# Kernel optimization log

Measured on AMD Instinct MI355X. Metric: run time of the kernel, lower is better.

The kernel has to match this reference:

```python
import jax, jax.numpy as jnp
import numpy as np

DN = ('NCHW', 'OIHW', 'NCHW')

def _conv(x, W, pad):
    return jax.lax.conv_general_dilated(x, W, (1, 1), [(pad, pad), (pad, pad)], dimension_numbers=DN)

def _cbs(x, W, s, b, pad):
    # Conv2d(bias=False) + folded BatchNorm (scale/bias) + SiLU
    y = _conv(x, W, pad) * s[None, :, None, None] + b[None, :, None, None]
    return y * jax.nn.sigmoid(y)

def _l2norm(x):
    n = jnp.sqrt(jnp.sum(x * x, axis=1, keepdims=True))
    return x / jnp.maximum(n, 1e-12)

def setup_inputs() -> dict:
    key = jax.random.key(0)
    ks = jax.random.split(key, 24)
    B, C, H, L, TD, NC = 16, 256, 64, 40, 768, 8
    EMB = (TD + NC * 2) // 2  # 392
    w = lambda k, sh: jax.random.normal(k, sh, jnp.float32) * 0.02
    img = jax.random.normal(ks[0], (B, C, H, H), jnp.float32)
    flang = jax.random.normal(ks[1], (B, L, TD), jnp.float32)
    lengths = jax.random.randint(ks[2], (B, 1), 5, L + 1)
    word_mask = (jnp.arange(L)[None, :] < lengths).astype(jnp.int32)
    return {
        'img': img, 'flang': flang, 'word_mask': word_mask, 'sigma_w': 0.1,
        'W1': w(ks[3], (EMB, TD)), 'b1': w(ks[4], (EMB,)),
        'W2': w(ks[5], (NC * 2, EMB)), 'b2': w(ks[6], (NC * 2,)),
        'Wv': w(ks[7], (C, C, 1, 1)), 'sv': jnp.ones((C,)), 'bv': w(ks[8], (C,)),
        'Wg': w(ks[9], (NC, NC, 1, 1)), 'sg': jnp.ones((NC,)), 'bg': w(ks[10], (NC,)),
        'Wb': w(ks[11], (NC, NC, 1, 1)), 'sb': jnp.ones((NC,)), 'bb': w(ks[12], (NC,)),
        'Wf1': w(ks[13], (C, C, 1, 1)), 'sf1': jnp.ones((C,)), 'bf1': w(ks[14], (C,)),
        'Wf2': w(ks[15], (C, C, 3, 3)), 'sf2': jnp.ones((C,)), 'bf2': w(ks[16], (C,)),
        'Wf3': w(ks[17], (C, C, 1, 1)), 'bf3': w(ks[18], (C,)),
        'Ws': w(ks[19], (NC, C, 3, 3)), 'bs': w(ks[20], (NC,)),
        'add_weight': jnp.zeros((), jnp.float32),
    }

def reference(img, flang, word_mask, sigma_w, W1, b1, W2, b2, Wv, sv, bv,
              Wg, sg, bg, Wb, sb, bb, Wf1, sf1, bf1, Wf2, sf2, bf2,
              Wf3, bf3, Ws, bs, add_weight):
    B, C, H = img.shape[0], img.shape[1], img.shape[2]
    nc = Wg.shape[0]
    map_visu = jnp.tanh(_cbs(img, Wv, sv, bv, 0))
    # ragged masked mean excluding first (CLS) and last (SEP) masked tokens
    m = word_mask.astype(jnp.float32)
    c = jnp.cumsum(m, axis=1)
    tot = c[:, -1:]
    inc = m * ((c > 1) & (c < tot)).astype(jnp.float32)  # [B,L]
    flang_avg = jnp.sum(flang * inc[:, :, None], axis=1) / jnp.sum(inc, axis=1, keepdims=True)
    map_flang = jax.nn.sigmoid((flang_avg @ W1.T + b1) @ W2.T + b2)  # [B,2*nc]
    maps = map_flang.reshape(B, nc, 2)
    sigma_x = sigma_w * H
    sig = _conv(img, Ws, 0) + bs[None, :, None, None]  # [B,nc,H-2,H-2]
    sigma_weight = jax.nn.sigmoid(jnp.mean(sig, axis=(2, 3), keepdims=True))  # [B,nc,1,1]
    sigma_y = sigma_x * sigma_weight
    yc = (maps[:, :, 0] * H).astype(jnp.int32).astype(jnp.float32)[:, :, None, None]
    xc = (maps[:, :, 1] * H).astype(jnp.int32).astype(jnp.float32)[:, :, None, None]
    gy = jnp.arange(H, dtype=jnp.float32)[None, None, :, None]
    gx = jnp.arange(H, dtype=jnp.float32)[None, None, None, :]
    weights = jnp.exp(-((gy - yc) ** 2 / (2.0 * sigma_y ** 2) + (gx - xc) ** 2 / (2.0 * sigma_x ** 2)))  # [B,nc,H,H]
    gamma = jnp.tanh(_cbs(weights, Wg, sg, bg, 0))
    beta = jnp.tanh(_cbs(weights, Wb, sb, bb, 0))
    g = jnp.mean(gamma, axis=1, keepdims=True)
    bmax = jnp.max(beta, axis=1, keepdims=True)
    v_film = _l2norm(g * map_visu + bmax)
    v_film = _cbs(v_film, Wf1, sf1, bf1, 0)
    v_film = _cbs(v_film, Wf2, sf2, bf2, 1)
    v_film = _conv(v_film, Wf3, 0) + bf3[None, :, None, None]
    aw = jnp.tanh(add_weight)
    v_add = (1.0 + aw) * img + (1.0 - aw) * v_film
    return _l2norm(v_add)
```

## Files before the change

kernel.cpp:

```cpp
#include <hip/hip_runtime.h>
#include <hip/hip_bf16.h>


#define DEVFN static __device__ __forceinline__

DEVFN float sigmoidf_(float x) { return 1.f / (1.f + expf(-x)); }
DEVFN float siluf_(float y) { return y / (1.f + __expf(-y)); }
DEVFN float tanh_fast_(float x) { return 1.f - 2.f / (__expf(2.f * x) + 1.f); }

typedef __attribute__((ext_vector_type(8))) short bf16x8;
typedef __attribute__((ext_vector_type(4))) float f32x4;

DEVFN unsigned short f2bf_(float f) {
    union { __hip_bfloat16 b; unsigned short u; } cv;
    cv.b = __float2bfloat16(f);
    return cv.u;
}
DEVFN float bf2f_(unsigned short u) {
    union { unsigned short u; __hip_bfloat16 b; } cv;
    cv.u = u;
    return __bfloat162float(cv.b);
}

DEVFN void async_cp16(const void* g, void* l) {
    __builtin_amdgcn_global_load_lds(
        (const __attribute__((address_space(1))) unsigned int*)g,
        (__attribute__((address_space(3))) unsigned int*)l, 16, 0, 0);
}

#define M1_LANG_END 16
#define M1_WSUM_END 1040
#define M1_GRID     1680

__global__ __launch_bounds__(256) void mega1_kernel(
        const float* __restrict__ Wv, const float* __restrict__ Wf1,
        const float* __restrict__ Wf3, const float* __restrict__ Wf2,
        short* __restrict__ WvB, short* __restrict__ W1B,
        short* __restrict__ W3B, short* __restrict__ WB2,
        float* __restrict__ zbuf,
        const float* __restrict__ img, float* __restrict__ S,
        const float* __restrict__ flang, const int* __restrict__ mask,
        const float* __restrict__ Wm1, const float* __restrict__ bm1,
        const float* __restrict__ Wm2, const float* __restrict__ bm2,
        float* __restrict__ ycxc) {
    __shared__ int   mlds[40];
    __shared__ float inc[40];
    __shared__ float isum;
    __shared__ __attribute__((aligned(16))) float fa[768];
    __shared__ float h[392];
    __shared__ float o16[16];
    int bid = blockIdx.x, t = threadIdx.x;
    int w = t >> 6, lane = t & 63;

    if (bid < M1_LANG_END) {
        int b = bid;
        if (t < 40) mlds[t] = mask[b * 40 + t];
        __syncthreads();
        if (t == 0) {
            float cum = 0.f;
            float tot = 0.f;
            for (int l = 0; l < 40; ++l) tot += (float)mlds[l];
            float sm = 0.f;
            for (int l = 0; l < 40; ++l) {
                float m = (float)mlds[l];
                cum += m;
                float v = (cum > 1.f && cum < tot) ? m : 0.f;
                inc[l] = v; sm += v;
            }
            isum = sm;
        }
        __syncthreads();
        {
            float rinv = 1.f / isum;
            for (int d = t; d < 768; d += 256) {
                float a = 0.f;
                const float* fp = flang + (size_t)(b * 40) * 768 + d;
                for (int l = 0; l < 40; ++l) a = fmaf(fp[(size_t)l * 768], inc[l], a);
                fa[d] = a * rinv;
            }
        }
        __syncthreads();
        {
            const float4* W14 = (const float4*)Wm1;
            const float4* fa4 = (const float4*)fa;
            for (int u = w; u < 392; u += 4) {
                float a = 0.f;
#pragma unroll
                for (int j = 0; j < 3; ++j) {
                    float4 wv = W14[(size_t)u * 192 + j * 64 + lane];
                    float4 fv = fa4[j * 64 + lane];
                    a = fmaf(wv.x, fv.x, a);
                    a = fmaf(wv.y, fv.y, a);
                    a = fmaf(wv.z, fv.z, a);
                    a = fmaf(wv.w, fv.w, a);
                }
#pragma unroll
                for (int m = 32; m; m >>= 1) a += __shfl_xor(a, m);
                if (lane == 0) h[u] = a + bm1[u];
            }
        }
        __syncthreads();
        {
#pragma unroll
            for (int q = 0; q < 4; ++q) {
                int u2 = w * 4 + q;
                float a = 0.f;
#pragma unroll
                for (int j = 0; j < 7; ++j) {
                    int k = j * 64 + lane;
                    if (k < 392) a = fmaf(h[k], Wm2[(size_t)u2 * 392 + k], a);
                }
#pragma unroll
                for (int m = 32; m; m >>= 1) a += __shfl_xor(a, m);
                if (lane == 0) o16[u2] = sigmoidf_(a + bm2[u2]);
            }
        }
        __syncthreads();
        if (t < 8) {
            ycxc[b * 8 + t]       = (float)(int)(o16[2 * t] * 64.f);
            ycxc[128 + b * 8 + t] = (float)(int)(o16[2 * t + 1] * 64.f);
        }
    } else if (bid < M1_WSUM_END) {
        int bc = (bid - M1_LANG_END) * 4 + w;
        const float4* p4 = (const float4*)(img + (size_t)bc * 4096);
        int lx2 = lane & 15;
        float s[9];
#pragma unroll
        for (int k = 0; k < 9; ++k) s[k] = 0.f;
#pragma unroll
        for (int i = 0; i < 16; ++i) {
            float4 v = p4[lane + i * 64];
            int y = (lane >> 4) + 4 * i;
            float sum4 = v.x + v.y + v.z + v.w;
            float p0 = (lx2 == 15) ? (v.x + v.y) : sum4;
            float p1 = sum4 - ((lx2 == 0) ? v.x : 0.f)
                            - ((lx2 == 15) ? v.w : 0.f);
            float p2 = (lx2 == 0) ? (v.z + v.w) : sum4;
            float ym0 = (y <= 61) ? 1.f : 0.f;
            float ym1 = (y >= 1 && y <= 62) ? 1.f : 0.f;
            float ym2 = (y >= 2) ? 1.f : 0.f;
            s[0] = fmaf(ym0, p0, s[0]); s[1] = fmaf(ym0, p1, s[1]); s[2] = fmaf(ym0, p2, s[2]);
            s[3] = fmaf(ym1, p0, s[3]); s[4] = fmaf(ym1, p1, s[4]); s[5] = fmaf(ym1, p2, s[5]);
            s[6] = fmaf(ym2, p0, s[6]); s[7] = fmaf(ym2, p1, s[7]); s[8] = fmaf(ym2, p2, s[8]);
        }
#pragma unroll
        for (int m = 32; m; m >>= 1)
#pragma unroll
            for (int k = 0; k < 9; ++k) s[k] += __shfl_xor(s[k], m);
        if (lane == 0) {
#pragma unroll
            for (int k = 0; k < 9; ++k) S[(size_t)bc * 9 + k] = s[k];
        }
    } else {
        int base = (bid - M1_WSUM_END) * 1024;
#pragma unroll
        for (int i = 0; i < 4; ++i) {
            int idx = base + i * 256 + t;
            if (idx < 8) zbuf[idx] = 0.f;
            if (idx < 65536) {
                int j    = idx & 7;
                int ln   = (idx >> 3) & 63;
                int coT  = (idx >> 9) & 15;
                int ci32 = (idx >> 13) & 7;
                int co = coT * 16 + (ln & 15);
                int ci = ci32 * 32 + ((ln >> 4) << 3) + j;
                int src = co * 256 + ci;
                WvB[idx] = (short)f2bf_(Wv[src]);
                W1B[idx] = (short)f2bf_(Wf1[src]);
                W3B[idx] = (short)f2bf_(Wf3[src]);
            }
            int oo = idx - 65536;
            if (oo >= 0 && oo < 589824) {
                int j    = oo & 7;
                int ln   = (oo >> 3) & 63;
                int coT  = (oo >> 9) & 15;
                int ci32 = (oo >> 13) & 7;
                int kk   = oo >> 16;
                int co = coT * 16 + (ln & 15);
                int ci = ci32 * 32 + ((ln >> 4) << 3) + j;
                WB2[oo] = (short)f2bf_(Wf2[(co * 256 + ci) * 9 + kk]);
            }
        }
    }
}

__global__ __launch_bounds__(256) void f01_kernel(
        const float* __restrict__ img, const short* __restrict__ wvb,
        const short* __restrict__ w1b,
        const float* __restrict__ sv, const float* __restrict__ bv,
        const float* __restrict__ s1, const float* __restrict__ b1,
        const float* __restrict__ S, const float* __restrict__ Ws,
        const float* __restrict__ bs, const float* __restrict__ ycxc,
        const float* __restrict__ sigma_w,
        const float* __restrict__ Wg, const float* __restrict__ sg,
        const float* __restrict__ bg,
        const float* __restrict__ Wb, const float* __restrict__ sb,
        const float* __restrict__ bb,
        __hip_bfloat16* __restrict__ outB) {
    __shared__ __attribute__((aligned(16))) short lA[64 * 264];
    __shared__ float invs[64];
    __shared__ float ls_sv[256], ls_bv[256], ls_s1[256], ls_b1[256];
    __shared__ float ls_g[64], ls_bm[64];
    __shared__ float sigw8[8];
    float* red = (float*)lA;
    float* pr  = (float*)lA;
    int blk = blockIdx.x, b = blk >> 6, y = blk & 63;
    int t = threadIdx.x, w = t >> 6, lane = t & 63;
    int lx = lane & 15, koct = lane >> 4;

    ls_sv[t] = sv[t]; ls_bv[t] = bv[t];
    ls_s1[t] = s1[t]; ls_b1[t] = b1[t];

    {
        float s9[9];
        const float* Sp = S + (size_t)(b * 256 + t) * 9;
#pragma unroll
        for (int k = 0; k < 9; ++k) s9[k] = Sp[k];
#pragma unroll
        for (int co = 0; co < 8; ++co) {
            const float* wp = Ws + (size_t)(co * 256 + t) * 9;
            float a = 0.f;
#pragma unroll
            for (int k = 0; k < 9; ++k) a = fmaf(wp[k], s9[k], a);
            red[co * 256 + t] = a;
        }
        __syncthreads();
        for (int st = 128; st > 0; st >>= 1) {
            if (t < st) {
#pragma unroll
                for (int co = 0; co < 8; ++co) red[co * 256 + t] += red[co * 256 + t + st];
            }
            __syncthreads();
        }
        if (t < 8) sigw8[t] = sigmoidf_(red[t * 256] / 3844.f + bs[t]);
        __syncthreads();
    }

    if (t < 64) {
        float sx = sigma_w[0] * 64.f;
        float wv8[8];
#pragma unroll
        for (int n = 0; n < 8; ++n) {
            float yc = ycxc[b * 8 + n], xc = ycxc[128 + b * 8 + n];
            float sy = sx * sigw8[n];
            float dy = (float)y - yc, dx = (float)t - xc;
            wv8[n] = expf(-(dy * dy / (2.f * sy * sy) + dx * dx / (2.f * sx * sx)));
        }
        float gacc = 0.f, bmax = -3.4e38f;
#pragma unroll
        for (int n = 0; n < 8; ++n) {
            float a1 = 0.f, a2 = 0.f;
#pragma unroll
            for (int m = 0; m < 8; ++m) {
                a1 = fmaf(Wg[n * 8 + m], wv8[m], a1);
                a2 = fmaf(Wb[n * 8 + m], wv8[m], a2);
            }
            float ga = tanhf(siluf_(a1 * sg[n] + bg[n]));
            float be = tanhf(siluf_(a2 * sb[n] + bb[n]));
            gacc += ga;
            bmax = fmaxf(bmax, be);
        }
        ls_g[t]  = gacc * 0.125f;
        ls_bm[t] = bmax;
    }

    {
        int x = t & 63, cg = t >> 6;
        const float* ib = img + (size_t)b * 1048576 + y * 64 + x;
#pragma unroll
        for (int c8 = 0; c8 < 8; ++c8) {
            int ci0 = cg * 64 + c8 * 8;
            unsigned short r[8];
#pragma unroll
            for (int j = 0; j < 8; ++j) r[j] = f2bf_(ib[(size_t)(ci0 + j) * 4096]);
            *(uint4*)&lA[x * 264 + ci0] = *(uint4*)r;
        }
    }
    f32x4 acc[4][4];
#pragma unroll
    for (int mi = 0; mi < 4; ++mi)
#pragma unroll
        for (int ni = 0; ni < 4; ++ni) acc[mi][ni] = (f32x4){0.f, 0.f, 0.f, 0.f};
    __syncthreads();

#pragma unroll
    for (int k32 = 0; k32 < 8; ++k32) {
        const short* wp = wvb + (((k32 * 16) + w * 4) * 64 + lane) * 8;
        bf16x8 bfr[4];
#pragma unroll
        for (int ni = 0; ni < 4; ++ni) bfr[ni] = *(const bf16x8*)(wp + ni * 512);
        bf16x8 afr[4];
#pragma unroll
        for (int mi = 0; mi < 4; ++mi)
            afr[mi] = *(const bf16x8*)&lA[(mi * 16 + lx) * 264 + k32 * 32 + koct * 8];
#pragma unroll
        for (int mi = 0; mi < 4; ++mi)
#pragma unroll
            for (int ni = 0; ni < 4; ++ni)
                acc[mi][ni] = __builtin_amdgcn_mfma_f32_16x16x32_bf16(afr[mi], bfr[ni], acc[mi][ni], 0, 0, 0);
    }
    __syncthreads();

#pragma unroll
    for (int mi = 0; mi < 4; ++mi)
#pragma unroll
        for (int rr = 0; rr < 4; ++rr) {
            int x = mi * 16 + koct * 4 + rr;
            float ps = 0.f;
#pragma unroll
            for (int ni = 0; ni < 4; ++ni) {
                int co = w * 64 + ni * 16 + lx;
                float yv = fmaf(acc[mi][ni][rr], ls_sv[co], ls_bv[co]);
                float mvv = tanh_fast_(siluf_(yv));
                float v = fmaf(ls_g[x], mvv, ls_bm[x]);
                acc[mi][ni][rr] = v;
                ps += v * v;
            }
            pr[x * 64 + w * 16 + lx] = ps;
        }
    __syncthreads();
    if (t < 64) {
        float s2 = 0.f;
        for (int q = 0; q < 64; ++q) s2 += pr[t * 64 + q];
        invs[t] = 1.f / fmaxf(sqrtf(s2), 1e-12f);
    }
    __syncthreads();

#pragma unroll
    for (int mi = 0; mi < 4; ++mi)
#pragma unroll
        for (int ni = 0; ni < 4; ++ni) {
            int co = w * 64 + ni * 16 + lx;
#pragma unroll
            for (int rr = 0; rr < 4; ++rr) {
                int x = mi * 16 + koct * 4 + rr;
                lA[x * 264 + co] = (short)f2bf_(acc[mi][ni][rr] * invs[x]);
            }
        }
#pragma unroll
    for (int mi = 0; mi < 4; ++mi)
#pragma unroll
        for (int ni = 0; ni < 4; ++ni) acc[mi][ni] = (f32x4){0.f, 0.f, 0.f, 0.f};
    __syncthreads();

#pragma unroll
    for (int k32 = 0; k32 < 8; ++k32) {
        const short* wp = w1b + (((k32 * 16) + w * 4) * 64 + lane) * 8;
        bf16x8 bfr[4];
#pragma unroll
        for (int ni = 0; ni < 4; ++ni) bfr[ni] = *(const bf16x8*)(wp + ni * 512);
        bf16x8 afr[4];
#pragma unroll
        for (int mi = 0; mi < 4; ++mi)
            afr[mi] = *(const bf16x8*)&lA[(mi * 16 + lx) * 264 + k32 * 32 + koct * 8];
#pragma unroll
        for (int mi = 0; mi < 4; ++mi)
#pragma unroll
            for (int ni = 0; ni < 4; ++ni)
                acc[mi][ni] = __builtin_amdgcn_mfma_f32_16x16x32_bf16(afr[mi], bfr[ni], acc[mi][ni], 0, 0, 0);
    }
    __syncthreads();

#pragma unroll
    for (int mi = 0; mi < 4; ++mi)
#pragma unroll
        for (int ni = 0; ni < 4; ++ni) {
            int co = w * 64 + ni * 16 + lx;
#pragma unroll
            for (int rr = 0; rr < 4; ++rr) {
                int x = mi * 16 + koct * 4 + rr;
                float yv = fmaf(acc[mi][ni][rr], ls_s1[co], ls_b1[co]);
                lA[x * 264 + co] = (short)f2bf_(siluf_(yv));
            }
        }
    __syncthreads();
    unsigned short* og = (unsigned short*)outB + (size_t)(b * 64 + y) * 16384;
#pragma unroll
    for (int it = 0; it < 8; ++it) {
        int e8 = t + it * 256;
        int x2 = e8 >> 5, c8 = e8 & 31;
        *(uint4*)(og + e8 * 8) = *(uint4*)&lA[x2 * 264 + c8 * 8];
    }
}

DEVFN void stage_chunk(const unsigned short* __restrict__ xg, short* ldsbuf,
                       const unsigned short* __restrict__ zbuf, int cc, int y0, int t) {
#pragma unroll
    for (int p = 0; p < 10; ++p) {
        int slot = t + p * 256;
        if (slot < 2376) {
            int r = slot / 594;
            int rem = slot - r * 594;
            int xp = rem / 9;
            int oct = rem - xp * 9;
            int ys = y0 + r - 1, xs = xp - 1;
            bool valid = (oct < 8) && (ys >= 0) && (ys < 64) && (xs >= 0) && (xs < 64);
            const unsigned short* gp = valid ? (xg + ((ys * 64 + xs) * 256 + cc * 64 + oct * 8))
                                             : zbuf;
            async_cp16(gp, ldsbuf + slot * 8);
        }
    }
}

__global__ __launch_bounds__(256, 2) void c3f_kernel(const __hip_bfloat16* __restrict__ xin,
                                                     const short* __restrict__ wb,
                                                     const float* __restrict__ sc,
                                                     const float* __restrict__ bi,
                                                     const float* __restrict__ zbufF,
                                                     const short* __restrict__ w3b,
                                                     const float* __restrict__ bf3,
                                                     const float* __restrict__ img,
                                                     const float* __restrict__ addw,
                                                     float* __restrict__ outF) {
    __shared__ __attribute__((aligned(16))) short lds[2][19008];
    __shared__ float pr2[256];
    __shared__ float invs[64];
    __shared__ float ls_b3[256];
    int blk = blockIdx.x;
    int b = blk >> 5, y0 = (blk & 31) * 2;
    int t = threadIdx.x;
    int w = t >> 6, lane = t & 63;
    int lx = lane & 15, koct = lane >> 4;
    const unsigned short* xg = (const unsigned short*)xin + (size_t)b * 1048576;
    const unsigned short* zbuf = (const unsigned short*)zbufF;
    ls_b3[t] = bf3[t];

    f32x4 acc[8][4];
#pragma unroll
    for (int mi = 0; mi < 8; ++mi)
#pragma unroll
        for (int ni = 0; ni < 4; ++ni) acc[mi][ni] = (f32x4){0.f, 0.f, 0.f, 0.f};

    stage_chunk(xg, lds[0], zbuf, 0, y0, t);
    __syncthreads();

    for (int cc = 0; cc < 4; ++cc) {
        short* cur = lds[cc & 1];
        if (cc < 3) stage_chunk(xg, lds[(cc + 1) & 1], zbuf, cc + 1, y0, t);
        for (int kk = 0; kk < 9; ++kk) {
            int ky = kk / 3, kx = kk - ky * 3;
#pragma unroll
            for (int k32 = 0; k32 < 2; ++k32) {
                const short* wp = wb + ((((kk * 8 + cc * 2 + k32) * 16) + w * 4) * 64 + lane) * 8;
                bf16x8 bfr[4];
#pragma unroll
                for (int ni = 0; ni < 4; ++ni)
                    bfr[ni] = *(const bf16x8*)(wp + ni * 512);
                bf16x8 afr[8];
#pragma unroll
                for (int mi = 0; mi < 8; ++mi) {
                    int row = mi >> 2, xb = (mi & 3) * 16;
                    afr[mi] = *(const bf16x8*)&cur[((row + ky) * 66 + xb + lx + kx) * 72 + k32 * 32 + koct * 8];
                }
#pragma unroll
                for (int mi = 0; mi < 8; ++mi)
#pragma unroll
                    for (int ni = 0; ni < 4; ++ni)
                        acc[mi][ni] = __builtin_amdgcn_mfma_f32_16x16x32_bf16(afr[mi], bfr[ni], acc[mi][ni], 0, 0, 0);
            }
        }
        __syncthreads();
    }

    float aw = tanhf(addw[0]);
    float ca = 1.f + aw, cb = 1.f - aw;
    short* ep  = &lds[0][0];
    short* wst = &lds[1][0];
#pragma unroll
    for (int r2 = 0; r2 < 2; ++r2) {
#pragma unroll
        for (int mi4 = 0; mi4 < 4; ++mi4) {
            int mi = r2 * 4 + mi4;
#pragma unroll
            for (int ni = 0; ni < 4; ++ni) {
                int co = w * 64 + ni * 16 + lx;
                float s = sc[co], bb2 = bi[co];
#pragma unroll
                for (int rr = 0; rr < 4; ++rr) {
                    int x = mi4 * 16 + koct * 4 + rr;
                    float yv = fmaf(acc[mi][ni][rr], s, bb2);
                    ep[x * 264 + co] = (short)f2bf_(siluf_(yv));
                }
            }
        }
        __syncthreads();
        f32x4 acc2[4][4];
#pragma unroll
        for (int mi = 0; mi < 4; ++mi)
#pragma unroll
            for (int ni = 0; ni < 4; ++ni) acc2[mi][ni] = (f32x4){0.f, 0.f, 0.f, 0.f};
#pragma unroll
        for (int k32 = 0; k32 < 8; ++k32) {
            const short* wp = w3b + (((k32 * 16) + w * 4) * 64 + lane) * 8;
            bf16x8 bfr[4];
#pragma unroll
            for (int ni = 0; ni < 4; ++ni) bfr[ni] = *(const bf16x8*)(wp + ni * 512);
            bf16x8 afr[4];
#pragma unroll
            for (int mi = 0; mi < 4; ++mi)
                afr[mi] = *(const bf16x8*)&ep[(mi * 16 + lx) * 264 + k32 * 32 + koct * 8];
#pragma unroll
            for (int mi = 0; mi < 4; ++mi)
#pragma unroll
                for (int ni = 0; ni < 4; ++ni)
                    acc2[mi][ni] = __builtin_amdgcn_mfma_f32_16x16x32_bf16(afr[mi], bfr[ni], acc2[mi][ni], 0, 0, 0);
        }
#pragma unroll
        for (int mi = 0; mi < 4; ++mi)
#pragma unroll
            for (int ni = 0; ni < 4; ++ni) {
                int co = w * 64 + ni * 16 + lx;
                float b3 = ls_b3[co];
#pragma unroll
                for (int rr = 0; rr < 4; ++rr) {
                    int x = mi * 16 + koct * 4 + rr;
                    wst[co * 66 + x] = (short)f2bf_(acc2[mi][ni][rr] + b3);
                }
            }
        __syncthreads();
        int x = t & 63, cg = t >> 6;
        const float* ip = img + (size_t)b * 1048576 + (size_t)(y0 + r2) * 64 + x;
        float ss = 0.f;
#pragma unroll 8
        for (int j = 0; j < 64; ++j) {
            int co = cg * 64 + j;
            float v = fmaf(cb, bf2f_((unsigned short)wst[co * 66 + x]), ca * ip[(size_t)co * 4096]);
            ss += v * v;
        }
        pr2[cg * 64 + x] = ss;
        __syncthreads();
        if (t < 64)
            invs[t] = 1.f / fmaxf(sqrtf(pr2[t] + pr2[64 + t] + pr2[128 + t] + pr2[192 + t]), 1e-12f);
        __syncthreads();
        float iv = invs[x];
        float* op = outF + (size_t)b * 1048576 + (size_t)(y0 + r2) * 64 + x;
#pragma unroll 8
        for (int j = 0; j < 64; ++j) {
            int co = cg * 64 + j;
            float v = fmaf(cb, bf2f_((unsigned short)wst[co * 66 + x]), ca * ip[(size_t)co * 4096]);
            op[(size_t)co * 4096] = v * iv;
        }
        __syncthreads();
    }
}

extern "C" void kernel_launch(void* const* d_in, const int* in_sizes, int n_in,
                              void* d_out, int out_size, void* d_ws, size_t ws_size,
                              hipStream_t stream) {
    const float* img     = (const float*)d_in[0];
    const float* flang   = (const float*)d_in[1];
    const int*   wmask   = (const int*)d_in[2];
    const float* sigma_w = (const float*)d_in[3];
    const float* W1      = (const float*)d_in[4];
    const float* b1      = (const float*)d_in[5];
    const float* W2      = (const float*)d_in[6];
    const float* b2      = (const float*)d_in[7];
    const float* Wv      = (const float*)d_in[8];
    const float* sv      = (const float*)d_in[9];
    const float* bv      = (const float*)d_in[10];
    const float* Wg      = (const float*)d_in[11];
    const float* sg      = (const float*)d_in[12];
    const float* bg      = (const float*)d_in[13];
    const float* Wb      = (const float*)d_in[14];
    const float* sb      = (const float*)d_in[15];
    const float* bb      = (const float*)d_in[16];
    const float* Wf1     = (const float*)d_in[17];
    const float* sf1     = (const float*)d_in[18];
    const float* bf1     = (const float*)d_in[19];
    const float* Wf2     = (const float*)d_in[20];
    const float* sf2     = (const float*)d_in[21];
    const float* bf2     = (const float*)d_in[22];
    const float* Wf3     = (const float*)d_in[23];
    const float* bf3     = (const float*)d_in[24];
    const float* Ws      = (const float*)d_in[25];
    const float* bs      = (const float*)d_in[26];
    const float* addw    = (const float*)d_in[27];
    float* out = (float*)d_out;
    float* ws  = (float*)d_ws;

    short* WvB  = (short*)ws;
    short* W1B  = (short*)(ws + 32768);
    short* W3B  = (short*)(ws + 65536);
    short* WB2  = (short*)(ws + 98304);
    float* ycxc = ws + 393216;
    float* S    = ws + 393472;
    float* zbuf = ws + 430336;
    __hip_bfloat16* bufB = (__hip_bfloat16*)(ws + 430352);

    mega1_kernel<<<M1_GRID, 256, 0, stream>>>(Wv, Wf1, Wf3, Wf2, WvB, W1B, W3B, WB2, zbuf,
                                              img, S, flang, wmask, W1, b1, W2, b2, ycxc);
    f01_kernel<<<1024, 256, 0, stream>>>(img, WvB, W1B, sv, bv, sf1, bf1,
                                         S, Ws, bs, ycxc, sigma_w,
                                         Wg, sg, bg, Wb, sb, bb, bufB);
    c3f_kernel<<<512, 256, 0, stream>>>(bufB, WB2, sf2, bf2, zbuf, W3B, bf3, img, addw, out);
}
```

Before: 407.9 us.

## Use 512-thread blocks with 32-channel K chunks in fused 3x3 conv kernel

Restructures the c3f kernel to run 8 waves per block, each owning 32 output channels instead of 64. Input channels are staged in chunks of 32 instead of 64, which shrinks the LDS footprint and halves per-wave accumulator registers. The epilogue is reworked for the smaller slice: the 1x1 conv and L2 norm now span 8 wave partials, and the LDS buffer is reused with an extra barrier. The aim is more waves in flight to hide latency, at the cost of more K-loop iterations, more barriers and less weight reuse per A-fragment load.

```diff
diff --git a/kernel.cpp b/kernel.cpp
--- a/kernel.cpp
+++ b/kernel.cpp
@@ -383,26 +383,26 @@
     }
 }
 
-DEVFN void stage_chunk(const unsigned short* __restrict__ xg, short* ldsbuf,
-                       const unsigned short* __restrict__ zbuf, int cc, int y0, int t) {
-#pragma unroll
-    for (int p = 0; p < 10; ++p) {
-        int slot = t + p * 256;
-        if (slot < 2376) {
-            int r = slot / 594;
-            int rem = slot - r * 594;
-            int xp = rem / 9;
-            int oct = rem - xp * 9;
+DEVFN void stage_chunk32(const unsigned short* __restrict__ xg, short* ldsbuf,
+                         const unsigned short* __restrict__ zbuf, int cc, int y0, int t) {
+#pragma unroll
+    for (int p = 0; p < 3; ++p) {
+        int slot = t + p * 512;
+        if (slot < 1320) {
+            int r = slot / 330;
+            int rem = slot - r * 330;
+            int xp = rem / 5;
+            int oct = rem - xp * 5;
             int ys = y0 + r - 1, xs = xp - 1;
-            bool valid = (oct < 8) && (ys >= 0) && (ys < 64) && (xs >= 0) && (xs < 64);
-            const unsigned short* gp = valid ? (xg + ((ys * 64 + xs) * 256 + cc * 64 + oct * 8))
+            bool valid = (oct < 4) && (ys >= 0) && (ys < 64) && (xs >= 0) && (xs < 64);
+            const unsigned short* gp = valid ? (xg + ((ys * 64 + xs) * 256 + cc * 32 + oct * 8))
                                              : zbuf;
             async_cp16(gp, ldsbuf + slot * 8);
         }
     }
 }
 
-__global__ __launch_bounds__(256, 2) void c3f_kernel(const __hip_bfloat16* __restrict__ xin,
+__global__ __launch_bounds__(512, 4) void c3f_kernel(const __hip_bfloat16* __restrict__ xin,
                                                      const short* __restrict__ wb,
                                                      const float* __restrict__ sc,
                                                      const float* __restrict__ bi,
@@ -412,8 +412,8 @@
                                                      const float* __restrict__ img,
                                                      const float* __restrict__ addw,
                                                      float* __restrict__ outF) {
-    __shared__ __attribute__((aligned(16))) short lds[2][19008];
-    __shared__ float pr2[256];
+    __shared__ __attribute__((aligned(16))) short lds[2][10560];
+    __shared__ float pr2[512];
     __shared__ float invs[64];
     __shared__ float ls_b3[256];
     int blk = blockIdx.x;
@@ -423,40 +423,36 @@
     int lx = lane & 15, koct = lane >> 4;
     const unsigned short* xg = (const unsigned short*)xin + (size_t)b * 1048576;
     const unsigned short* zbuf = (const unsigned short*)zbufF;
-    ls_b3[t] = bf3[t];
-
-    f32x4 acc[8][4];
+    if (t < 256) ls_b3[t] = bf3[t];
+
+    f32x4 acc[8][2];
 #pragma unroll
     for (int mi = 0; mi < 8; ++mi)
 #pragma unroll
-        for (int ni = 0; ni < 4; ++ni) acc[mi][ni] = (f32x4){0.f, 0.f, 0.f, 0.f};
-
-    stage_chunk(xg, lds[0], zbuf, 0, y0, t);
-    __syncthreads();
-
-    for (int cc = 0; cc < 4; ++cc) {
+        for (int ni = 0; ni < 2; ++ni) acc[mi][ni] = (f32x4){0.f, 0.f, 0.f, 0.f};
+
+    stage_chunk32(xg, lds[0], zbuf, 0, y0, t);
+    __syncthreads();
+
+    for (int cc = 0; cc < 8; ++cc) {
         short* cur = lds[cc & 1];
-        if (cc < 3) stage_chunk(xg, lds[(cc + 1) & 1], zbuf, cc + 1, y0, t);
+        if (cc < 7) stage_chunk32(xg, lds[(cc + 1) & 1], zbuf, cc + 1, y0, t);
         for (int kk = 0; kk < 9; ++kk) {
             int ky = kk / 3, kx = kk - ky * 3;
-#pragma unroll
-            for (int k32 = 0; k32 < 2; ++k32) {
-                const short* wp = wb + ((((kk * 8 + cc * 2 + k32) * 16) + w * 4) * 64 + lane) * 8;
-                bf16x8 bfr[4];
-#pragma unroll
-                for (int ni = 0; ni < 4; ++ni)
-                    bfr[ni] = *(const bf16x8*)(wp + ni * 512);
-                bf16x8 afr[8];
-#pragma unroll
-                for (int mi = 0; mi < 8; ++mi) {
-                    int row = mi >> 2, xb = (mi & 3) * 16;
-                    afr[mi] = *(const bf16x8*)&cur[((row + ky) * 66 + xb + lx + kx) * 72 + k32 * 32 + koct * 8];
+            const short* wp = wb + (((kk * 8 + cc) * 16 + w * 2) * 64 + lane) * 8;
+            bf16x8 bfr0 = *(const bf16x8*)wp;
+            bf16x8 bfr1 = *(const bf16x8*)(wp + 512);
+#pragma unroll
+            for (int half = 0; half < 2; ++half) {
+                bf16x8 afr[4];
+#pragma unroll
+                for (int m4 = 0; m4 < 4; ++m4)
+                    afr[m4] = *(const bf16x8*)&cur[((half + ky) * 66 + m4 * 16 + lx + kx) * 40 + koct * 8];
+#pragma unroll
+                for (int m4 = 0; m4 < 4; ++m4) {
+                    acc[half * 4 + m4][0] = __builtin_amdgcn_mfma_f32_16x16x32_bf16(afr[m4], bfr0, acc[half * 4 + m4][0], 0, 0, 0);
+                    acc[half * 4 + m4][1] = __builtin_amdgcn_mfma_f32_16x16x32_bf16(afr[m4], bfr1, acc[half * 4 + m4][1], 0, 0, 0);
                 }
-#pragma unroll
-                for (int mi = 0; mi < 8; ++mi)
-#pragma unroll
-                    for (int ni = 0; ni < 4; ++ni)
-                        acc[mi][ni] = __builtin_amdgcn_mfma_f32_16x16x32_bf16(afr[mi], bfr[ni], acc[mi][ni], 0, 0, 0);
             }
         }
         __syncthreads();
@@ -465,51 +461,49 @@
     float aw = tanhf(addw[0]);
     float ca = 1.f + aw, cb = 1.f - aw;
     short* ep  = &lds[0][0];
-    short* wst = &lds[1][0];
+    short* wst = &lds[0][0];
 #pragma unroll
     for (int r2 = 0; r2 < 2; ++r2) {
 #pragma unroll
-        for (int mi4 = 0; mi4 < 4; ++mi4) {
-            int mi = r2 * 4 + mi4;
-#pragma unroll
-            for (int ni = 0; ni < 4; ++ni) {
-                int co = w * 64 + ni * 16 + lx;
+        for (int mi4 = 0; mi4 < 4; ++mi4)
+#pragma unroll
+            for (int ni = 0; ni < 2; ++ni) {
+                int co = w * 32 + ni * 16 + lx;
                 float s = sc[co], bb2 = bi[co];
 #pragma unroll
                 for (int rr = 0; rr < 4; ++rr) {
                     int x = mi4 * 16 + koct * 4 + rr;
-                    float yv = fmaf(acc[mi][ni][rr], s, bb2);
+                    float yv = fmaf(acc[r2 * 4 + mi4][ni][rr], s, bb2);
                     ep[x * 264 + co] = (short)f2bf_(siluf_(yv));
                 }
             }
-        }
-        __syncthreads();
-        f32x4 acc2[4][4];
+        __syncthreads();
+        f32x4 acc2[4][2];
 #pragma unroll
         for (int mi = 0; mi < 4; ++mi)
 #pragma unroll
-            for (int ni = 0; ni < 4; ++ni) acc2[mi][ni] = (f32x4){0.f, 0.f, 0.f, 0.f};
+            for (int ni = 0; ni < 2; ++ni) acc2[mi][ni] = (f32x4){0.f, 0.f, 0.f, 0.f};
 #pragma unroll
         for (int k32 = 0; k32 < 8; ++k32) {
-            const short* wp = w3b + (((k32 * 16) + w * 4) * 64 + lane) * 8;
-            bf16x8 bfr[4];
-#pragma unroll
-            for (int ni = 0; ni < 4; ++ni) bfr[ni] = *(const bf16x8*)(wp + ni * 512);
+            const short* wp = w3b + ((k32 * 16 + w * 2) * 64 + lane) * 8;
+            bf16x8 b0 = *(const bf16x8*)wp;
+            bf16x8 b1 = *(const bf16x8*)(wp + 512);
             bf16x8 afr[4];
 #pragma unroll
             for (int mi = 0; mi < 4; ++mi)
                 afr[mi] = *(const bf16x8*)&ep[(mi * 16 + lx) * 264 + k32 * 32 + koct * 8];
 #pragma unroll
-            for (int mi = 0; mi < 4; ++mi)
-#pragma unroll
-                for (int ni = 0; ni < 4; ++ni)
-                    acc2[mi][ni] = __builtin_amdgcn_mfma_f32_16x16x32_bf16(afr[mi], bfr[ni], acc2[mi][ni], 0, 0, 0);
-        }
+            for (int mi = 0; mi < 4; ++mi) {
+                acc2[mi][0] = __builtin_amdgcn_mfma_f32_16x16x32_bf16(afr[mi], b0, acc2[mi][0], 0, 0, 0);
+                acc2[mi][1] = __builtin_amdgcn_mfma_f32_16x16x32_bf16(afr[mi], b1, acc2[mi][1], 0, 0, 0);
+            }
+        }
+        __syncthreads();
 #pragma unroll
         for (int mi = 0; mi < 4; ++mi)
 #pragma unroll
-            for (int ni = 0; ni < 4; ++ni) {
-                int co = w * 64 + ni * 16 + lx;
+            for (int ni = 0; ni < 2; ++ni) {
+                int co = w * 32 + ni * 16 + lx;
                 float b3 = ls_b3[co];
 #pragma unroll
                 for (int rr = 0; rr < 4; ++rr) {
@@ -522,21 +516,25 @@
         const float* ip = img + (size_t)b * 1048576 + (size_t)(y0 + r2) * 64 + x;
         float ss = 0.f;
 #pragma unroll 8
-        for (int j = 0; j < 64; ++j) {
-            int co = cg * 64 + j;
+        for (int j = 0; j < 32; ++j) {
+            int co = cg * 32 + j;
             float v = fmaf(cb, bf2f_((unsigned short)wst[co * 66 + x]), ca * ip[(size_t)co * 4096]);
             ss += v * v;
         }
         pr2[cg * 64 + x] = ss;
         __syncthreads();
-        if (t < 64)
-            invs[t] = 1.f / fmaxf(sqrtf(pr2[t] + pr2[64 + t] + pr2[128 + t] + pr2[192 + t]), 1e-12f);
+        if (t < 64) {
+            float s2 = 0.f;
+#pragma unroll
+            for (int q = 0; q < 8; ++q) s2 += pr2[q * 64 + t];
+            invs[t] = 1.f / fmaxf(sqrtf(s2), 1e-12f);
+        }
         __syncthreads();
         float iv = invs[x];
         float* op = outF + (size_t)b * 1048576 + (size_t)(y0 + r2) * 64 + x;
 #pragma unroll 8
-        for (int j = 0; j < 64; ++j) {
-            int co = cg * 64 + j;
+        for (int j = 0; j < 32; ++j) {
+            int co = cg * 32 + j;
             float v = fmaf(cb, bf2f_((unsigned short)wst[co * 66 + x]), ca * ip[(size_t)co * 4096]);
             op[(size_t)co * 4096] = v * iv;
         }
@@ -592,5 +590,5 @@
     f01_kernel<<<1024, 256, 0, stream>>>(img, WvB, W1B, sv, bv, sf1, bf1,
                                          S, Ws, bs, ycxc, sigma_w,
                                          Wg, sg, bg, Wb, sb, bb, bufB);
-    c3f_kernel<<<512, 256, 0, stream>>>(bufB, WB2, sf2, bf2, zbuf, W3B, bf3, img, addw, out);
-}
+    c3f_kernel<<<512, 512, 0, stream>>>(bufB, WB2, sf2, bf2, zbuf, W3B, bf3, img, addw, out);
+}
```

New measurement: 456.8 us. 12.0% more time.
